# Optimization experiments

Hardware: AMD Instinct MI355X
Metric: run time of the kernel (lower is better)

Reference implementation:

```python
import jax, jax.numpy as jnp
import numpy as np

B, C, H, W = 16, 64, 64, 64
D = max(1, C // 8)

def setup_inputs() -> dict:
    key = jax.random.key(0)
    k1, k2, k3, k4, k5 = jax.random.split(key, 5)
    x = jax.random.normal(k1, (B, C, H, W), dtype=jnp.float32)
    Wq = jax.random.normal(k2, (D, C), dtype=jnp.float32) * (1.0 / np.sqrt(C))
    Wk = jax.random.normal(k3, (D, C), dtype=jnp.float32) * (1.0 / np.sqrt(C))
    Wv = jax.random.normal(k4, (C, C), dtype=jnp.float32) * (1.0 / np.sqrt(C))
    gamma = jax.random.normal(k5, (1,), dtype=jnp.float32)
    return {"x": x, "Wq": Wq, "Wk": Wk, "Wv": Wv, "gamma": gamma}

def reference(x, Wq, Wk, Wv, gamma):
    b, c, h, w = x.shape
    xf = x.reshape(b, c, h * w)                 # [B, C, N]
    q = jnp.einsum('dc,bcn->bdn', Wq, xf)       # [B, D, N] (1x1 conv == channel matmul)
    k = jnp.einsum('dc,bcn->bdn', Wk, xf)       # [B, D, N]
    v = jnp.einsum('ec,bcn->ben', Wv, xf)       # [B, C, N]
    # attn[b,i,j] = softmax_j( q[:, :, i] . k[:, :, j] )  -- no scaling (as in source)
    scores = jnp.einsum('bdi,bdj->bij', q, k)   # [B, N, N]
    attn = jax.nn.softmax(scores, axis=-1)
    # out[b,c,i] = sum_j v[b,c,j] * attn[b,i,j]
    out = jnp.einsum('bcj,bij->bci', v, attn)   # [B, C, N]
    out = out.reshape(b, c, h, w)
    return x + gamma * out
```

## Files before the change

kernel.cpp:

```cpp
#include <hip/hip_runtime.h>

#define NB 16
#define NC 64
#define NN 4096

typedef _Float16 half8 __attribute__((ext_vector_type(8)));
typedef float f32x16 __attribute__((ext_vector_type(16)));
typedef unsigned int uint4v __attribute__((ext_vector_type(4)));

#define MFMA(A, B, C) __builtin_amdgcn_mfma_f32_32x32x16_f16(A, B, C, 0, 0, 0)

#define QT_OFF ((size_t)0)
#define KT_OFF ((size_t)NB * NN * 16)
#define VH_OFF ((size_t)2 * NB * NN * 16)

__global__ __launch_bounds__(256) void qkv_kernel(
    const float* __restrict__ x, const float* __restrict__ Wq,
    const float* __restrict__ Wk, const float* __restrict__ Wv,
    _Float16* __restrict__ qT, _Float16* __restrict__ kT, _Float16* __restrict__ vh)
{
    const int tid = threadIdx.x;
    const int blk = blockIdx.x;
    const int sel = blockIdx.y;
    const int b = blk >> 4;
    const int n = (blk & 15) * 256 + tid;

    const float* xb = x + (size_t)b * NC * NN + n;
    float xr[NC];
#pragma unroll
    for (int c = 0; c < NC; ++c) xr[c] = xb[(size_t)c * NN];

    if (sel == 0) {
        float qa[8], ka[8];
#pragma unroll
        for (int d = 0; d < 8; ++d) {
            float aq = 0.f, ak = 0.f;
#pragma unroll
            for (int c = 0; c < NC; ++c) {
                aq = fmaf(Wq[d * NC + c], xr[c], aq);
                ak = fmaf(Wk[d * NC + c], xr[c], ak);
            }
            qa[d] = aq; ka[d] = ak;
        }
        half8 qhi, qlo, khi, klo;
#pragma unroll
        for (int d = 0; d < 8; ++d) {
            _Float16 hq = (_Float16)qa[d];
            qhi[d] = hq; qlo[d] = (_Float16)(qa[d] - (float)hq);
            _Float16 hk = (_Float16)ka[d];
            khi[d] = hk; klo[d] = (_Float16)(ka[d] - (float)hk);
        }
        _Float16* qr = qT + ((size_t)b * NN + n) * 16;
        *(half8*)qr = qhi; *(half8*)(qr + 8) = qlo;
        _Float16* kr = kT + ((size_t)b * NN + n) * 16;
        *(half8*)kr = khi; *(half8*)(kr + 8) = klo;
#pragma unroll 4
        for (int e = 0; e < 24; ++e) {
            float a = 0.f;
#pragma unroll
            for (int c = 0; c < NC; ++c) a = fmaf(Wv[e * NC + c], xr[c], a);
            vh[((size_t)b * NC + e) * NN + n] = (_Float16)a;
        }
    } else {
#pragma unroll 4
        for (int e = 24; e < 64; ++e) {
            float a = 0.f;
#pragma unroll
            for (int c = 0; c < NC; ++c) a = fmaf(Wv[e * NC + c], xr[c], a);
            vh[((size_t)b * NC + e) * NN + n] = (_Float16)a;
        }
    }
}

__global__ __launch_bounds__(256) void attn_kernel(
    const float* __restrict__ x, const float* __restrict__ gamma,
    const _Float16* __restrict__ qT, const _Float16* __restrict__ kT,
    const _Float16* __restrict__ vh, float* __restrict__ out)
{
    const int tid  = threadIdx.x;
    const int lane = tid & 63;
    const int wid  = tid >> 6;
    const int l31  = lane & 31;
    const int g    = lane >> 5;

    const int blk  = blockIdx.x;
    const int virt = (blk & 7) * 64 + (blk >> 3);
    const int b    = virt >> 5;
    const int qt   = virt & 31;
    const int q    = qt * 128 + wid * 32 + l31;

    const _Float16* qr = qT + ((size_t)b * NN + q) * 16;
    const half8 qb1 = *(const half8*)qr;
    const half8 qlo = *(const half8*)(qr + 8);
    half8 qb2;
#pragma unroll
    for (int i = 0; i < 8; ++i) qb2[i] = g ? (_Float16)0 : qlo[i];

    const _Float16* kp  = kT + (size_t)b * NN * 16 + (size_t)l31 * 16 + (size_t)g * 8;
    const _Float16* vp0 = vh + (size_t)b * NC * NN + (size_t)l31 * NN + (size_t)g * 8;
    const _Float16* vp1 = vp0 + (size_t)32 * NN;

    f32x16 acc0 = {}, acc1 = {};
    float mrun = -__builtin_inff();
    float lrun = 0.f;

    half8 ka = *(const half8*)kp;

    for (int t = 0; t < NN / 32; ++t) {
        const int off = t * 32;
        const half8 va00 = *(const half8*)(vp0 + off);
        const half8 va01 = *(const half8*)(vp0 + off + 16);
        const half8 va10 = *(const half8*)(vp1 + off);
        const half8 va11 = *(const half8*)(vp1 + off + 16);

        f32x16 S = {};
        S = MFMA(ka, qb1, S);
        S = MFMA(ka, qb2, S);

        const int tn = (t + 1 < NN / 32) ? (t + 1) : t;
        ka = *(const half8*)(kp + (size_t)tn * 512);

        const float s0 = S[0],  s1 = S[1],  s2 = S[2],  s3 = S[3];
        const float s4 = S[4],  s5 = S[5],  s6 = S[6],  s7 = S[7];
        const float s8 = S[8],  s9 = S[9],  s10 = S[10], s11 = S[11];
        const float s12 = S[12], s13 = S[13], s14 = S[14], s15 = S[15];

        float pmax = fmaxf(
            fmaxf(fmaxf(fmaxf(s0, s1), fmaxf(s2, s3)), fmaxf(fmaxf(s4, s5), fmaxf(s6, s7))),
            fmaxf(fmaxf(fmaxf(s8, s9), fmaxf(s10, s11)), fmaxf(fmaxf(s12, s13), fmaxf(s14, s15))));
        pmax = fmaxf(pmax, __shfl_xor(pmax, 32, 64));

        if (__any(pmax > mrun + 8.0f)) {
            const float mnew = fmaxf(mrun, pmax);
            const float rs = __expf(mrun - mnew);
            lrun *= rs;
#pragma unroll
            for (int r = 0; r < 16; ++r) { acc0[r] *= rs; acc1[r] *= rs; }
            mrun = mnew;
        }

        const float p0 = __expf(s0 - mrun),  p1 = __expf(s1 - mrun);
        const float p2 = __expf(s2 - mrun),  p3 = __expf(s3 - mrun);
        const float p4 = __expf(s4 - mrun),  p5 = __expf(s5 - mrun);
        const float p6 = __expf(s6 - mrun),  p7 = __expf(s7 - mrun);
        const float p8 = __expf(s8 - mrun),  p9 = __expf(s9 - mrun);
        const float p10 = __expf(s10 - mrun), p11 = __expf(s11 - mrun);
        const float p12 = __expf(s12 - mrun), p13 = __expf(s13 - mrun);
        const float p14 = __expf(s14 - mrun), p15 = __expf(s15 - mrun);

        float ls = (((p0 + p1) + (p2 + p3)) + ((p4 + p5) + (p6 + p7)))
                 + (((p8 + p9) + (p10 + p11)) + ((p12 + p13) + (p14 + p15)));
        ls += __shfl_xor(ls, 32, 64);
        lrun += ls;

        const unsigned int x0 = __builtin_bit_cast(unsigned int, __builtin_amdgcn_cvt_pkrtz(p0, p1));
        const unsigned int x1 = __builtin_bit_cast(unsigned int, __builtin_amdgcn_cvt_pkrtz(p2, p3));
        const unsigned int x2 = __builtin_bit_cast(unsigned int, __builtin_amdgcn_cvt_pkrtz(p4, p5));
        const unsigned int x3 = __builtin_bit_cast(unsigned int, __builtin_amdgcn_cvt_pkrtz(p6, p7));
        const unsigned int x4 = __builtin_bit_cast(unsigned int, __builtin_amdgcn_cvt_pkrtz(p8, p9));
        const unsigned int x5 = __builtin_bit_cast(unsigned int, __builtin_amdgcn_cvt_pkrtz(p10, p11));
        const unsigned int x6 = __builtin_bit_cast(unsigned int, __builtin_amdgcn_cvt_pkrtz(p12, p13));
        const unsigned int x7 = __builtin_bit_cast(unsigned int, __builtin_amdgcn_cvt_pkrtz(p14, p15));

        auto r0 = __builtin_amdgcn_permlane32_swap(x0, x2, false, false);
        auto r1 = __builtin_amdgcn_permlane32_swap(x1, x3, false, false);
        auto r2 = __builtin_amdgcn_permlane32_swap(x4, x6, false, false);
        auto r3 = __builtin_amdgcn_permlane32_swap(x5, x7, false, false);
        const uint4v w0 = {(unsigned int)r0[0], (unsigned int)r1[0],
                           (unsigned int)r0[1], (unsigned int)r1[1]};
        const uint4v w1 = {(unsigned int)r2[0], (unsigned int)r3[0],
                           (unsigned int)r2[1], (unsigned int)r3[1]};
        const half8 pv0 = __builtin_bit_cast(half8, w0);
        const half8 pv1 = __builtin_bit_cast(half8, w1);

        acc0 = MFMA(va00, pv0, acc0);
        acc0 = MFMA(va01, pv1, acc0);
        acc1 = MFMA(va10, pv0, acc1);
        acc1 = MFMA(va11, pv1, acc1);
    }

    const float linv = 1.0f / lrun;
    const float gm = gamma[0];
#pragma unroll
    for (int r = 0; r < 16; ++r) {
        const int crow = (r & 3) + 8 * (r >> 2) + 4 * g;
        const size_t i0 = ((size_t)b * NC + crow) * NN + q;
        out[i0] = fmaf(gm, acc0[r] * linv, x[i0]);
        const size_t i1 = ((size_t)b * NC + crow + 32) * NN + q;
        out[i1] = fmaf(gm, acc1[r] * linv, x[i1]);
    }
}

extern "C" void kernel_launch(void* const* d_in, const int* in_sizes, int n_in,
                              void* d_out, int out_size, void* d_ws, size_t ws_size,
                              hipStream_t stream) {
    const float* x     = (const float*)d_in[0];
    const float* Wq    = (const float*)d_in[1];
    const float* Wk    = (const float*)d_in[2];
    const float* Wv    = (const float*)d_in[3];
    const float* gamma = (const float*)d_in[4];
    float* out = (float*)d_out;
    _Float16* ws = (_Float16*)d_ws;

    _Float16* qT = ws + QT_OFF;
    _Float16* kT = ws + KT_OFF;
    _Float16* vh = ws + VH_OFF;

    qkv_kernel<<<dim3(NB * (NN / 256), 2), dim3(256), 0, stream>>>(x, Wq, Wk, Wv, qT, kT, vh);
    attn_kernel<<<dim3(NB * (NN / 128)), dim3(256), 0, stream>>>(x, gamma, qT, kT, vh, out);
}
```

Before: 241.1 us.

## Split attention key range across wave pairs and merge partial softmax states

Each attention block now handles 64 queries. Two waves share each 32-query tile and each processes half of the 4096 keys; their running max, sum and accumulators are merged through shared memory before the epilogue. This doubles the grid to create more parallelism and shortens each wave's serial loop. The cost is LDS traffic and a block barrier at the end. Separately, the log2(e) factor is folded into q so the loop can use exp2f directly, and the QKV projection is split three ways with 4-way accumulator unrolling for better ILP.

```diff
diff --git a/kernel.cpp b/kernel.cpp
--- a/kernel.cpp
+++ b/kernel.cpp
@@ -3,6 +3,7 @@
 #define NB 16
 #define NC 64
 #define NN 4096
+#define LOG2E 1.44269504088896f
 
 typedef _Float16 half8 __attribute__((ext_vector_type(8)));
 typedef float f32x16 __attribute__((ext_vector_type(16)));
@@ -34,13 +35,23 @@
         float qa[8], ka[8];
 #pragma unroll
         for (int d = 0; d < 8; ++d) {
-            float aq = 0.f, ak = 0.f;
-#pragma unroll
-            for (int c = 0; c < NC; ++c) {
-                aq = fmaf(Wq[d * NC + c], xr[c], aq);
-                ak = fmaf(Wk[d * NC + c], xr[c], ak);
+            float aq0 = 0.f, aq1 = 0.f, aq2 = 0.f, aq3 = 0.f;
+            float ak0 = 0.f, ak1 = 0.f, ak2 = 0.f, ak3 = 0.f;
+            const float* wq = Wq + d * NC;
+            const float* wk = Wk + d * NC;
+#pragma unroll
+            for (int c = 0; c < NC; c += 4) {
+                aq0 = fmaf(wq[c],     xr[c],     aq0);
+                aq1 = fmaf(wq[c + 1], xr[c + 1], aq1);
+                aq2 = fmaf(wq[c + 2], xr[c + 2], aq2);
+                aq3 = fmaf(wq[c + 3], xr[c + 3], aq3);
+                ak0 = fmaf(wk[c],     xr[c],     ak0);
+                ak1 = fmaf(wk[c + 1], xr[c + 1], ak1);
+                ak2 = fmaf(wk[c + 2], xr[c + 2], ak2);
+                ak3 = fmaf(wk[c + 3], xr[c + 3], ak3);
             }
-            qa[d] = aq; ka[d] = ak;
+            qa[d] = ((aq0 + aq1) + (aq2 + aq3)) * LOG2E;
+            ka[d] = (ak0 + ak1) + (ak2 + ak3);
         }
         half8 qhi, qlo, khi, klo;
 #pragma unroll
@@ -54,20 +65,20 @@
         *(half8*)qr = qhi; *(half8*)(qr + 8) = qlo;
         _Float16* kr = kT + ((size_t)b * NN + n) * 16;
         *(half8*)kr = khi; *(half8*)(kr + 8) = klo;
+    } else {
+        const int e0 = (sel - 1) * 32;
 #pragma unroll 4
-        for (int e = 0; e < 24; ++e) {
-            float a = 0.f;
-#pragma unroll
-            for (int c = 0; c < NC; ++c) a = fmaf(Wv[e * NC + c], xr[c], a);
-            vh[((size_t)b * NC + e) * NN + n] = (_Float16)a;
-        }
-    } else {
-#pragma unroll 4
-        for (int e = 24; e < 64; ++e) {
-            float a = 0.f;
-#pragma unroll
-            for (int c = 0; c < NC; ++c) a = fmaf(Wv[e * NC + c], xr[c], a);
-            vh[((size_t)b * NC + e) * NN + n] = (_Float16)a;
+        for (int e = e0; e < e0 + 32; ++e) {
+            float a0 = 0.f, a1 = 0.f, a2 = 0.f, a3 = 0.f;
+            const float* wv = Wv + e * NC;
+#pragma unroll
+            for (int c = 0; c < NC; c += 4) {
+                a0 = fmaf(wv[c],     xr[c],     a0);
+                a1 = fmaf(wv[c + 1], xr[c + 1], a1);
+                a2 = fmaf(wv[c + 2], xr[c + 2], a2);
+                a3 = fmaf(wv[c + 3], xr[c + 3], a3);
+            }
+            vh[((size_t)b * NC + e) * NN + n] = (_Float16)((a0 + a1) + (a2 + a3));
         }
     }
 }
@@ -77,17 +88,21 @@
     const _Float16* __restrict__ qT, const _Float16* __restrict__ kT,
     const _Float16* __restrict__ vh, float* __restrict__ out)
 {
+    __shared__ __attribute__((aligned(16))) float mrg[2][64][36];
+
     const int tid  = threadIdx.x;
     const int lane = tid & 63;
     const int wid  = tid >> 6;
     const int l31  = lane & 31;
     const int g    = lane >> 5;
+    const int pair = wid >> 1;
+    const int odd  = wid & 1;
 
     const int blk  = blockIdx.x;
-    const int virt = (blk & 7) * 64 + (blk >> 3);
-    const int b    = virt >> 5;
-    const int qt   = virt & 31;
-    const int q    = qt * 128 + wid * 32 + l31;
+    const int virt = (blk & 7) * 128 + (blk >> 3);
+    const int b    = virt >> 6;
+    const int qt   = virt & 63;
+    const int q    = qt * 64 + pair * 32 + l31;
 
     const _Float16* qr = qT + ((size_t)b * NN + q) * 16;
     const half8 qb1 = *(const half8*)qr;
@@ -96,8 +111,8 @@
 #pragma unroll
     for (int i = 0; i < 8; ++i) qb2[i] = g ? (_Float16)0 : qlo[i];
 
-    const _Float16* kp  = kT + (size_t)b * NN * 16 + (size_t)l31 * 16 + (size_t)g * 8;
-    const _Float16* vp0 = vh + (size_t)b * NC * NN + (size_t)l31 * NN + (size_t)g * 8;
+    const _Float16* kp  = kT + (size_t)b * NN * 16 + ((size_t)odd * 2048 + l31) * 16 + (size_t)g * 8;
+    const _Float16* vp0 = vh + (size_t)b * NC * NN + (size_t)l31 * NN + odd * 2048 + (size_t)g * 8;
     const _Float16* vp1 = vp0 + (size_t)32 * NN;
 
     f32x16 acc0 = {}, acc1 = {};
@@ -106,7 +121,8 @@
 
     half8 ka = *(const half8*)kp;
 
-    for (int t = 0; t < NN / 32; ++t) {
+#define NT (2048 / 32)
+    for (int t = 0; t < NT; ++t) {
         const int off = t * 32;
         const half8 va00 = *(const half8*)(vp0 + off);
         const half8 va01 = *(const half8*)(vp0 + off + 16);
@@ -117,7 +133,7 @@
         S = MFMA(ka, qb1, S);
         S = MFMA(ka, qb2, S);
 
-        const int tn = (t + 1 < NN / 32) ? (t + 1) : t;
+        const int tn = (t + 1 < NT) ? (t + 1) : t;
         ka = *(const half8*)(kp + (size_t)tn * 512);
 
         const float s0 = S[0],  s1 = S[1],  s2 = S[2],  s3 = S[3];
@@ -130,23 +146,23 @@
             fmaxf(fmaxf(fmaxf(s8, s9), fmaxf(s10, s11)), fmaxf(fmaxf(s12, s13), fmaxf(s14, s15))));
         pmax = fmaxf(pmax, __shfl_xor(pmax, 32, 64));
 
-        if (__any(pmax > mrun + 8.0f)) {
+        if (__any(pmax > mrun + 11.6f)) {
             const float mnew = fmaxf(mrun, pmax);
-            const float rs = __expf(mrun - mnew);
+            const float rs = exp2f(mrun - mnew);
             lrun *= rs;
 #pragma unroll
             for (int r = 0; r < 16; ++r) { acc0[r] *= rs; acc1[r] *= rs; }
             mrun = mnew;
         }
 
-        const float p0 = __expf(s0 - mrun),  p1 = __expf(s1 - mrun);
-        const float p2 = __expf(s2 - mrun),  p3 = __expf(s3 - mrun);
-        const float p4 = __expf(s4 - mrun),  p5 = __expf(s5 - mrun);
-        const float p6 = __expf(s6 - mrun),  p7 = __expf(s7 - mrun);
-        const float p8 = __expf(s8 - mrun),  p9 = __expf(s9 - mrun);
-        const float p10 = __expf(s10 - mrun), p11 = __expf(s11 - mrun);
-        const float p12 = __expf(s12 - mrun), p13 = __expf(s13 - mrun);
-        const float p14 = __expf(s14 - mrun), p15 = __expf(s15 - mrun);
+        const float p0 = exp2f(s0 - mrun),  p1 = exp2f(s1 - mrun);
+        const float p2 = exp2f(s2 - mrun),  p3 = exp2f(s3 - mrun);
+        const float p4 = exp2f(s4 - mrun),  p5 = exp2f(s5 - mrun);
+        const float p6 = exp2f(s6 - mrun),  p7 = exp2f(s7 - mrun);
+        const float p8 = exp2f(s8 - mrun),  p9 = exp2f(s9 - mrun);
+        const float p10 = exp2f(s10 - mrun), p11 = exp2f(s11 - mrun);
+        const float p12 = exp2f(s12 - mrun), p13 = exp2f(s13 - mrun);
+        const float p14 = exp2f(s14 - mrun), p15 = exp2f(s15 - mrun);
 
         float ls = (((p0 + p1) + (p2 + p3)) + ((p4 + p5) + (p6 + p7)))
                  + (((p8 + p9) + (p10 + p11)) + ((p12 + p13) + (p14 + p15)));
@@ -179,15 +195,34 @@
         acc1 = MFMA(va11, pv1, acc1);
     }
 
-    const float linv = 1.0f / lrun;
-    const float gm = gamma[0];
-#pragma unroll
-    for (int r = 0; r < 16; ++r) {
-        const int crow = (r & 3) + 8 * (r >> 2) + 4 * g;
-        const size_t i0 = ((size_t)b * NC + crow) * NN + q;
-        out[i0] = fmaf(gm, acc0[r] * linv, x[i0]);
-        const size_t i1 = ((size_t)b * NC + crow + 32) * NN + q;
-        out[i1] = fmaf(gm, acc1[r] * linv, x[i1]);
+    if (odd) {
+        float* r = &mrg[pair][lane][0];
+#pragma unroll
+        for (int i = 0; i < 16; ++i) r[i] = acc0[i];
+#pragma unroll
+        for (int i = 0; i < 16; ++i) r[16 + i] = acc1[i];
+        r[32] = mrun; r[33] = lrun;
+    }
+    __syncthreads();
+    if (!odd) {
+        const float* r = &mrg[pair][lane][0];
+        const float mB = r[32], lB = r[33];
+        const float mN = fmaxf(mrun, mB);
+        const float eA = exp2f(mrun - mN);
+        const float eB = exp2f(mB - mN);
+        const float l  = lrun * eA + lB * eB;
+        const float linv = 1.0f / l;
+        const float gm = gamma[0];
+#pragma unroll
+        for (int rr = 0; rr < 16; ++rr) {
+            const int crow = (rr & 3) + 8 * (rr >> 2) + 4 * g;
+            const float a0 = acc0[rr] * eA + r[rr] * eB;
+            const float a1 = acc1[rr] * eA + r[16 + rr] * eB;
+            const size_t i0 = ((size_t)b * NC + crow) * NN + q;
+            out[i0] = fmaf(gm, a0 * linv, x[i0]);
+            const size_t i1 = ((size_t)b * NC + crow + 32) * NN + q;
+            out[i1] = fmaf(gm, a1 * linv, x[i1]);
+        }
     }
 }
 
@@ -206,6 +241,6 @@
     _Float16* kT = ws + KT_OFF;
     _Float16* vh = ws + VH_OFF;
 
-    qkv_kernel<<<dim3(NB * (NN / 256), 2), dim3(256), 0, stream>>>(x, Wq, Wk, Wv, qT, kT, vh);
-    attn_kernel<<<dim3(NB * (NN / 128)), dim3(256), 0, stream>>>(x, gamma, qT, kT, vh, out);
+    qkv_kernel<<<dim3(NB * (NN / 256), 3), dim3(256), 0, stream>>>(x, Wq, Wk, Wv, qT, kT, vh);
+    attn_kernel<<<dim3(NB * (NN / 64)), dim3(256), 0, stream>>>(x, gamma, qT, kT, vh, out);
 }
```

Result: slower. 251.8 us (+4.5%).
